# Kernel optimization log

Measured on AMD Instinct MI355X. Metric: run time of the kernel, lower is better.

Reference implementation:

```python
import jax, jax.numpy as jnp
import numpy as np

N, P, D = 262144, 128, 64
EPS = 1e-5
NEG = -1e30


def setup_inputs() -> dict:
    key = jax.random.key(0)
    ks = jax.random.split(key, 12)
    feature = jax.random.normal(ks[0], (N, D), jnp.float32)
    feature_geo = jax.random.normal(ks[1], (N, D), jnp.float32)
    xyz = jax.random.uniform(ks[2], (N, 3), jnp.float32)
    centers = jax.random.uniform(ks[3], (3,), jnp.float32)
    plane_center = jax.random.uniform(ks[4], (P, 3), jnp.float32)
    nrm = jax.random.normal(ks[5], (P, 3), jnp.float32)
    plane_normal = nrm / jnp.linalg.norm(nrm, axis=1, keepdims=True)
    lo = 0.3 * jax.random.uniform(ks[6], (P, 3), jnp.float32)
    hi = 0.5 + 0.5 * jax.random.uniform(ks[7], (P, 3), jnp.float32)
    # exactly two active axes per plane (one axis of the aabb is zeroed)
    ax = jnp.arange(P) % 3
    keep = (jnp.arange(3)[None, :] != ax[:, None]).astype(jnp.float32)
    plane_xyz_min = lo * keep
    plane_xyz_max = hi * keep
    w1 = 0.05 * jax.random.normal(ks[8], (2 * D, D), jnp.float32)
    b1 = jnp.zeros((D,), jnp.float32)
    w2 = 0.05 * jax.random.normal(ks[9], (D, D), jnp.float32)
    b2 = jnp.zeros((D,), jnp.float32)
    w3 = 0.05 * jax.random.normal(ks[10], (D, 1), jnp.float32)
    b3 = jnp.zeros((1,), jnp.float32)
    g1 = jnp.ones((D,), jnp.float32); be1 = jnp.zeros((D,), jnp.float32)
    m1 = jnp.zeros((D,), jnp.float32); v1 = jnp.ones((D,), jnp.float32)
    g2 = jnp.ones((D,), jnp.float32); be2 = jnp.zeros((D,), jnp.float32)
    m2 = jnp.zeros((D,), jnp.float32); v2 = jnp.ones((D,), jnp.float32)
    return dict(feature=feature, feature_geo=feature_geo, xyz=xyz, centers=centers,
                plane_center=plane_center, plane_normal=plane_normal,
                plane_xyz_min=plane_xyz_min, plane_xyz_max=plane_xyz_max,
                w1=w1, b1=b1, g1=g1, be1=be1, m1=m1, v1=v1,
                w2=w2, b2=b2, g2=g2, be2=be2, m2=m2, v2=v2,
                w3=w3, b3=b3)


def _bn(x, g, b, m, v):
    return (x - m) * (g * jax.lax.rsqrt(v + EPS)) + b


def reference(feature, feature_geo, xyz, centers, plane_center, plane_normal,
              plane_xyz_min, plane_xyz_max, w1, b1, g1, be1, m1, v1,
              w2, b2, g2, be2, m2, v2, w3, b3):
    clouds = xyz + centers                                   # [N,3]
    f = jnp.concatenate([feature, feature_geo], axis=1)      # [N,2D]
    # 1x1 conv MLP == per-point matmul (fc1 -> fc2 with BN+ReLU, fc3)
    h1 = jax.nn.relu(_bn(f @ w1 + b1, g1, be1, m1, v1))      # [N,D]
    h2 = jax.nn.relu(_bn(h1 @ w2 + b2, g2, be2, m2, v2))     # [N,D]
    scores = jax.nn.relu(h2 @ w3 + b3)[:, 0]                 # [N]
    # per-plane aabb mask over the two active axes (xyz_max != 0)
    active = plane_xyz_max != 0                              # [P,3]
    in_rng = (clouds[None] >= plane_xyz_min[:, None]) & (clouds[None] < plane_xyz_max[:, None])
    range_mask = jnp.all(in_rng | ~active[:, None, :], axis=-1)   # [P,N]
    # point-to-plane distance: |(clouds - center) . normal|
    dots = clouds @ plane_normal.T                           # [N,P]
    offs = jnp.sum(plane_center * plane_normal, axis=1)      # [P]
    dist = jnp.abs(dots - offs[None, :]).T                   # [P,N]
    mask = range_mask & (dist < 0.1)                         # [P,N]
    sig = jax.nn.sigmoid(scores)                             # [N]
    on_mask = mask & (sig > 0.5)[None, :]
    off_mask = mask & (sig <= 0.5)[None, :]

    def pool(m):  # masked max-pool of fc2 features over points of one plane
        val = jnp.max(jnp.where(m[:, None], h2, NEG), axis=0)     # [D]
        return jnp.where(jnp.any(m), val, 0.0)

    on_feat = jax.lax.map(pool, on_mask)                     # [P,D]
    off_feat = jax.lax.map(pool, off_mask)                   # [P,D]
    scores_masked = jnp.where(mask, scores[None, :], 0.0)    # [P,N]
    return scores_masked, mask, on_mask, off_mask, on_feat, off_feat
```

## Files before the change

kernel.cpp:

```cpp
#include <hip/hip_runtime.h>
#include <hip/hip_bf16.h>
#include <math.h>

#define NPTS 262144
#define NP   128
#define DD   64
#define NWORDS (NPTS / 64)

__global__ __launch_bounds__(256) void prep_kernel(
    const float* __restrict__ plane_center, const float* __restrict__ plane_normal,
    const float* __restrict__ pmin, const float* __restrict__ pmax,
    float* __restrict__ packed, float* __restrict__ out_feats)
{
    const int t = threadIdx.x;
    out_feats[blockIdx.x * 256 + t] = 0.0f;
    if (blockIdx.x == 0 && t < NP) {
        float n0 = plane_normal[t*3+0], n1 = plane_normal[t*3+1], n2 = plane_normal[t*3+2];
        float c0 = plane_center[t*3+0], c1 = plane_center[t*3+1], c2 = plane_center[t*3+2];
        float off = (c0*n0 + c1*n1) + c2*n2;
        float4* pp = reinterpret_cast<float4*>(packed) + t * 3;
        pp[0] = make_float4(n0, n1, n2, off);
        pp[1] = make_float4(pmin[t*3+0], pmin[t*3+1], pmin[t*3+2], 0.0f);
        pp[2] = make_float4(pmax[t*3+0], pmax[t*3+1], pmax[t*3+2], 0.0f);
    }
}

__global__ __launch_bounds__(256) void mlp1_kernel(
    const float* __restrict__ feature, const float* __restrict__ feature_geo,
    const float* __restrict__ w1, const float* __restrict__ b1,
    const float* __restrict__ g1, const float* __restrict__ be1,
    const float* __restrict__ m1, const float* __restrict__ v1,
    float* __restrict__ h1_out)
{
    const int n = blockIdx.x * 256 + threadIdx.x;
    float acc[DD];
#pragma unroll
    for (int j = 0; j < DD; ++j) acc[j] = 0.0f;

    const float4* fA = reinterpret_cast<const float4*>(feature) + (size_t)n * 16;
#pragma unroll 1
    for (int q = 0; q < 16; ++q) {
        const float4 fv = fA[q];
        const float* wr = w1 + q * 4 * DD;
#pragma unroll
        for (int j = 0; j < DD; ++j) acc[j] = fmaf(fv.x, wr[j], acc[j]);
#pragma unroll
        for (int j = 0; j < DD; ++j) acc[j] = fmaf(fv.y, wr[DD + j], acc[j]);
#pragma unroll
        for (int j = 0; j < DD; ++j) acc[j] = fmaf(fv.z, wr[2 * DD + j], acc[j]);
#pragma unroll
        for (int j = 0; j < DD; ++j) acc[j] = fmaf(fv.w, wr[3 * DD + j], acc[j]);
    }
    const float4* fB = reinterpret_cast<const float4*>(feature_geo) + (size_t)n * 16;
    const float* w1b = w1 + DD * DD;
#pragma unroll 1
    for (int q = 0; q < 16; ++q) {
        const float4 fv = fB[q];
        const float* wr = w1b + q * 4 * DD;
#pragma unroll
        for (int j = 0; j < DD; ++j) acc[j] = fmaf(fv.x, wr[j], acc[j]);
#pragma unroll
        for (int j = 0; j < DD; ++j) acc[j] = fmaf(fv.y, wr[DD + j], acc[j]);
#pragma unroll
        for (int j = 0; j < DD; ++j) acc[j] = fmaf(fv.z, wr[2 * DD + j], acc[j]);
#pragma unroll
        for (int j = 0; j < DD; ++j) acc[j] = fmaf(fv.w, wr[3 * DD + j], acc[j]);
    }
#pragma unroll
    for (int j = 0; j < DD; ++j) {
        float sc = g1[j] * (1.0f / sqrtf(v1[j] + 1e-5f));
        float h  = fmaf(acc[j] + b1[j] - m1[j], sc, be1[j]);
        acc[j] = fmaxf(h, 0.0f);
    }
    float4* o = reinterpret_cast<float4*>(h1_out) + (size_t)n * 16;
#pragma unroll
    for (int q = 0; q < 16; ++q)
        o[q] = make_float4(acc[4*q+0], acc[4*q+1], acc[4*q+2], acc[4*q+3]);
}

__global__ __launch_bounds__(256) void mlp2_kernel(
    const float* __restrict__ h1_in,
    const float* __restrict__ w2, const float* __restrict__ b2,
    const float* __restrict__ g2, const float* __restrict__ be2,
    const float* __restrict__ m2, const float* __restrict__ v2,
    const float* __restrict__ w3, const float* __restrict__ b3,
    float* __restrict__ h2_out, float* __restrict__ scores_out)
{
    const int n = blockIdx.x * 256 + threadIdx.x;
    float acc[DD];
#pragma unroll
    for (int j = 0; j < DD; ++j) acc[j] = 0.0f;

    const float4* fA = reinterpret_cast<const float4*>(h1_in) + (size_t)n * 16;
#pragma unroll 1
    for (int q = 0; q < 16; ++q) {
        const float4 fv = fA[q];
        const float* wr = w2 + q * 4 * DD;
#pragma unroll
        for (int j = 0; j < DD; ++j) acc[j] = fmaf(fv.x, wr[j], acc[j]);
#pragma unroll
        for (int j = 0; j < DD; ++j) acc[j] = fmaf(fv.y, wr[DD + j], acc[j]);
#pragma unroll
        for (int j = 0; j < DD; ++j) acc[j] = fmaf(fv.z, wr[2 * DD + j], acc[j]);
#pragma unroll
        for (int j = 0; j < DD; ++j) acc[j] = fmaf(fv.w, wr[3 * DD + j], acc[j]);
    }
    float s = 0.0f;
#pragma unroll
    for (int j = 0; j < DD; ++j) {
        float sc = g2[j] * (1.0f / sqrtf(v2[j] + 1e-5f));
        float h  = fmaf(acc[j] + b2[j] - m2[j], sc, be2[j]);
        h = fmaxf(h, 0.0f);
        acc[j] = h;
        s = fmaf(h, w3[j], s);
    }
    s += b3[0];
    float4* o = reinterpret_cast<float4*>(h2_out) + (size_t)n * 16;
#pragma unroll
    for (int q = 0; q < 16; ++q)
        o[q] = make_float4(acc[4*q+0], acc[4*q+1], acc[4*q+2], acc[4*q+3]);
    scores_out[n] = fmaxf(s, 0.0f);
}

__global__ __launch_bounds__(256) void mask_kernel(
    const float* __restrict__ xyz, const float* __restrict__ centers,
    const float* __restrict__ packed,
    const float* __restrict__ scores,
    float* __restrict__ out_sm, float* __restrict__ out_mask,
    float* __restrict__ out_on, float* __restrict__ out_off,
    unsigned long long* __restrict__ hitOn, unsigned long long* __restrict__ hitOff)
{
    const int t = threadIdx.x;
    const int n = blockIdx.x * 256 + t;
    const float c0 = xyz[n*3+0] + centers[0];
    const float c1 = xyz[n*3+1] + centers[1];
    const float c2 = xyz[n*3+2] + centers[2];
    const float s  = scores[n];
    const bool on  = (0.5f + 0.5f * tanhf(0.5f * s)) > 0.5f;
    const int lane = t & 63;
    const int word = n >> 6;

    const float4* pp = reinterpret_cast<const float4*>(packed);
#pragma unroll 1
    for (int p = 0; p < NP; ++p) {
        float4 nrm = pp[p*3+0];
        float4 mn  = pp[p*3+1];
        float4 mx  = pp[p*3+2];
        float d = fabsf(fmaf(c2, nrm.z, fmaf(c1, nrm.y, c0 * nrm.x)) - nrm.w);
        bool ok0 = (mx.x == 0.0f) | ((c0 >= mn.x) & (c0 < mx.x));
        bool ok1 = (mx.y == 0.0f) | ((c1 >= mn.y) & (c1 < mx.y));
        bool ok2 = (mx.z == 0.0f) | ((c2 >= mn.z) & (c2 < mx.z));
        bool mk  = ok0 & ok1 & ok2 & (d < 0.1f);
        size_t idx = (size_t)p * NPTS + n;
        out_sm[idx]   = mk ? s : 0.0f;
        out_mask[idx] = mk ? 1.0f : 0.0f;
        bool mon  = mk & on;
        bool moff = mk & (!on);
        out_on[idx]  = mon  ? 1.0f : 0.0f;
        out_off[idx] = moff ? 1.0f : 0.0f;
        unsigned long long bOn  = __ballot(mon);
        unsigned long long bOff = __ballot(moff);
        if (lane == 0) {
            hitOn [(size_t)p * NWORDS + word] = bOn;
            hitOff[(size_t)p * NWORDS + word] = bOff;
        }
    }
}

__global__ __launch_bounds__(256) void pool_kernel(
    const float* __restrict__ h2,
    const unsigned long long* __restrict__ hitOn,
    const unsigned long long* __restrict__ hitOff,
    int* __restrict__ out_feats_i)
{
    __shared__ float tile[128 * DD];
    __shared__ unsigned long long bm[2][NP][2];
    const int t = threadIdx.x;
    const int lane = t & 63;
    const int wv = t >> 6;

    float accOn[32], accOff[32];
#pragma unroll
    for (int i = 0; i < 32; ++i) { accOn[i] = 0.0f; accOff[i] = 0.0f; }

    for (int cc = 0; cc < 4; ++cc) {
        const int chunk = blockIdx.x * 4 + cc;
        const int base  = chunk * 128;
        const float4* src = reinterpret_cast<const float4*>(h2 + (size_t)base * DD);
        float4* dst = reinterpret_cast<float4*>(tile);
#pragma unroll
        for (int q = 0; q < 8; ++q) dst[t + q * 256] = src[t + q * 256];
        {
            const int p = t & 127;
            const int half = t >> 7;
            const unsigned long long* hsrc = half ? hitOff : hitOn;
            const int w0 = chunk * 2;
            bm[half][p][0] = hsrc[(size_t)p * NWORDS + w0 + 0];
            bm[half][p][1] = hsrc[(size_t)p * NWORDS + w0 + 1];
        }
        __syncthreads();

#pragma unroll
        for (int i = 0; i < 32; ++i) {
            const int p = wv * 32 + i;
            unsigned long long m;
            m = bm[0][p][0];
            while (m) { int nn = __builtin_ctzll(m); m &= m - 1;
                        accOn[i]  = fmaxf(accOn[i],  tile[nn * DD + lane]); }
            m = bm[0][p][1];
            while (m) { int nn = __builtin_ctzll(m); m &= m - 1;
                        accOn[i]  = fmaxf(accOn[i],  tile[(64 + nn) * DD + lane]); }
            m = bm[1][p][0];
            while (m) { int nn = __builtin_ctzll(m); m &= m - 1;
                        accOff[i] = fmaxf(accOff[i], tile[nn * DD + lane]); }
            m = bm[1][p][1];
            while (m) { int nn = __builtin_ctzll(m); m &= m - 1;
                        accOff[i] = fmaxf(accOff[i], tile[(64 + nn) * DD + lane]); }
        }
        __syncthreads();
    }
#pragma unroll
    for (int i = 0; i < 32; ++i) {
        const int p = wv * 32 + i;
        if (accOn[i]  != 0.0f) atomicMax(&out_feats_i[p * DD + lane],            __float_as_int(accOn[i]));
        if (accOff[i] != 0.0f) atomicMax(&out_feats_i[NP * DD + p * DD + lane],  __float_as_int(accOff[i]));
    }
}

extern "C" void kernel_launch(void* const* d_in, const int* in_sizes, int n_in,
                              void* d_out, int out_size, void* d_ws, size_t ws_size,
                              hipStream_t stream) {
    const float* feature      = (const float*)d_in[0];
    const float* feature_geo  = (const float*)d_in[1];
    const float* xyz          = (const float*)d_in[2];
    const float* centers      = (const float*)d_in[3];
    const float* plane_center = (const float*)d_in[4];
    const float* plane_normal = (const float*)d_in[5];
    const float* pmin         = (const float*)d_in[6];
    const float* pmax         = (const float*)d_in[7];
    const float* w1 = (const float*)d_in[8];
    const float* b1 = (const float*)d_in[9];
    const float* g1 = (const float*)d_in[10];
    const float* be1 = (const float*)d_in[11];
    const float* m1 = (const float*)d_in[12];
    const float* v1 = (const float*)d_in[13];
    const float* w2 = (const float*)d_in[14];
    const float* b2 = (const float*)d_in[15];
    const float* g2 = (const float*)d_in[16];
    const float* be2 = (const float*)d_in[17];
    const float* m2 = (const float*)d_in[18];
    const float* v2 = (const float*)d_in[19];
    const float* w3 = (const float*)d_in[20];
    const float* b3 = (const float*)d_in[21];

    float* out = (float*)d_out;
    const size_t PN = (size_t)NP * NPTS;
    float* out_sm    = out;
    float* out_mask  = out + PN;
    float* out_on    = out + 2 * PN;
    float* out_off   = out + 3 * PN;
    float* out_feats = out + 4 * PN;

    float* h1     = (float*)d_ws;
    float* h2     = h1 + (size_t)NPTS * DD;
    float* scores = h2 + (size_t)NPTS * DD;
    unsigned long long* hitOn  = (unsigned long long*)(scores + NPTS);
    unsigned long long* hitOff = hitOn + (size_t)NP * NWORDS;
    float* packed = (float*)(hitOff + (size_t)NP * NWORDS);

    prep_kernel<<<64, 256, 0, stream>>>(
        plane_center, plane_normal, pmin, pmax, packed, out_feats);
    mlp1_kernel<<<NPTS / 256, 256, 0, stream>>>(
        feature, feature_geo, w1, b1, g1, be1, m1, v1, h1);
    mlp2_kernel<<<NPTS / 256, 256, 0, stream>>>(
        h1, w2, b2, g2, be2, m2, v2, w3, b3, h2, scores);
    mask_kernel<<<NPTS / 256, 256, 0, stream>>>(
        xyz, centers, packed, scores,
        out_sm, out_mask, out_on, out_off, hitOn, hitOff);
    pool_kernel<<<512, 256, 0, stream>>>(h2, hitOn, hitOff, (int*)out_feats);
}
```

Measured before the change: 869.4 us.

## Fuse both MLP layers and mask generation into a single per-point kernel

Merges the two MLP kernels and the mask kernel into one kernel, so the first hidden layer and the score stay in registers instead of passing through global memory. This removes a large intermediate write/read and two launches. The cost is higher register pressure from holding two 64-float arrays at once, which may cause spills or lower occupancy during the store-heavy mask loop.

```diff
diff --git a/kernel.cpp b/kernel.cpp
--- a/kernel.cpp
+++ b/kernel.cpp
@@ -25,85 +25,82 @@
     }
 }
 
-__global__ __launch_bounds__(256) void mlp1_kernel(
+__global__ __launch_bounds__(256) void fused_kernel(
     const float* __restrict__ feature, const float* __restrict__ feature_geo,
+    const float* __restrict__ xyz, const float* __restrict__ centers,
+    const float* __restrict__ packed,
     const float* __restrict__ w1, const float* __restrict__ b1,
     const float* __restrict__ g1, const float* __restrict__ be1,
     const float* __restrict__ m1, const float* __restrict__ v1,
-    float* __restrict__ h1_out)
-{
-    const int n = blockIdx.x * 256 + threadIdx.x;
-    float acc[DD];
-#pragma unroll
-    for (int j = 0; j < DD; ++j) acc[j] = 0.0f;
-
-    const float4* fA = reinterpret_cast<const float4*>(feature) + (size_t)n * 16;
-#pragma unroll 1
-    for (int q = 0; q < 16; ++q) {
-        const float4 fv = fA[q];
-        const float* wr = w1 + q * 4 * DD;
-#pragma unroll
-        for (int j = 0; j < DD; ++j) acc[j] = fmaf(fv.x, wr[j], acc[j]);
-#pragma unroll
-        for (int j = 0; j < DD; ++j) acc[j] = fmaf(fv.y, wr[DD + j], acc[j]);
-#pragma unroll
-        for (int j = 0; j < DD; ++j) acc[j] = fmaf(fv.z, wr[2 * DD + j], acc[j]);
-#pragma unroll
-        for (int j = 0; j < DD; ++j) acc[j] = fmaf(fv.w, wr[3 * DD + j], acc[j]);
-    }
-    const float4* fB = reinterpret_cast<const float4*>(feature_geo) + (size_t)n * 16;
-    const float* w1b = w1 + DD * DD;
-#pragma unroll 1
-    for (int q = 0; q < 16; ++q) {
-        const float4 fv = fB[q];
-        const float* wr = w1b + q * 4 * DD;
-#pragma unroll
-        for (int j = 0; j < DD; ++j) acc[j] = fmaf(fv.x, wr[j], acc[j]);
-#pragma unroll
-        for (int j = 0; j < DD; ++j) acc[j] = fmaf(fv.y, wr[DD + j], acc[j]);
-#pragma unroll
-        for (int j = 0; j < DD; ++j) acc[j] = fmaf(fv.z, wr[2 * DD + j], acc[j]);
-#pragma unroll
-        for (int j = 0; j < DD; ++j) acc[j] = fmaf(fv.w, wr[3 * DD + j], acc[j]);
-    }
-#pragma unroll
-    for (int j = 0; j < DD; ++j) {
-        float sc = g1[j] * (1.0f / sqrtf(v1[j] + 1e-5f));
-        float h  = fmaf(acc[j] + b1[j] - m1[j], sc, be1[j]);
-        acc[j] = fmaxf(h, 0.0f);
-    }
-    float4* o = reinterpret_cast<float4*>(h1_out) + (size_t)n * 16;
-#pragma unroll
-    for (int q = 0; q < 16; ++q)
-        o[q] = make_float4(acc[4*q+0], acc[4*q+1], acc[4*q+2], acc[4*q+3]);
-}
-
-__global__ __launch_bounds__(256) void mlp2_kernel(
-    const float* __restrict__ h1_in,
     const float* __restrict__ w2, const float* __restrict__ b2,
     const float* __restrict__ g2, const float* __restrict__ be2,
     const float* __restrict__ m2, const float* __restrict__ v2,
     const float* __restrict__ w3, const float* __restrict__ b3,
-    float* __restrict__ h2_out, float* __restrict__ scores_out)
+    float* __restrict__ h2_out,
+    float* __restrict__ out_sm, float* __restrict__ out_mask,
+    float* __restrict__ out_on, float* __restrict__ out_off,
+    unsigned long long* __restrict__ hitOn, unsigned long long* __restrict__ hitOff)
 {
-    const int n = blockIdx.x * 256 + threadIdx.x;
+    const int t = threadIdx.x;
+    const int n = blockIdx.x * 256 + t;
+
+    const float c0 = xyz[n*3+0] + centers[0];
+    const float c1 = xyz[n*3+1] + centers[1];
+    const float c2 = xyz[n*3+2] + centers[2];
+
     float acc[DD];
 #pragma unroll
     for (int j = 0; j < DD; ++j) acc[j] = 0.0f;
 
-    const float4* fA = reinterpret_cast<const float4*>(h1_in) + (size_t)n * 16;
+    const float4* fA = reinterpret_cast<const float4*>(feature) + (size_t)n * 16;
 #pragma unroll 1
     for (int q = 0; q < 16; ++q) {
         const float4 fv = fA[q];
+        const float* wr = w1 + q * 4 * DD;
+#pragma unroll
+        for (int j = 0; j < DD; ++j) acc[j] = fmaf(fv.x, wr[j], acc[j]);
+#pragma unroll
+        for (int j = 0; j < DD; ++j) acc[j] = fmaf(fv.y, wr[DD + j], acc[j]);
+#pragma unroll
+        for (int j = 0; j < DD; ++j) acc[j] = fmaf(fv.z, wr[2 * DD + j], acc[j]);
+#pragma unroll
+        for (int j = 0; j < DD; ++j) acc[j] = fmaf(fv.w, wr[3 * DD + j], acc[j]);
+    }
+    const float4* fB = reinterpret_cast<const float4*>(feature_geo) + (size_t)n * 16;
+    const float* w1b = w1 + DD * DD;
+#pragma unroll 1
+    for (int q = 0; q < 16; ++q) {
+        const float4 fv = fB[q];
+        const float* wr = w1b + q * 4 * DD;
+#pragma unroll
+        for (int j = 0; j < DD; ++j) acc[j] = fmaf(fv.x, wr[j], acc[j]);
+#pragma unroll
+        for (int j = 0; j < DD; ++j) acc[j] = fmaf(fv.y, wr[DD + j], acc[j]);
+#pragma unroll
+        for (int j = 0; j < DD; ++j) acc[j] = fmaf(fv.z, wr[2 * DD + j], acc[j]);
+#pragma unroll
+        for (int j = 0; j < DD; ++j) acc[j] = fmaf(fv.w, wr[3 * DD + j], acc[j]);
+    }
+    float h1[DD];
+#pragma unroll
+    for (int j = 0; j < DD; ++j) {
+        float sc = g1[j] * (1.0f / sqrtf(v1[j] + 1e-5f));
+        float h  = fmaf(acc[j] + b1[j] - m1[j], sc, be1[j]);
+        h1[j] = fmaxf(h, 0.0f);
+        acc[j] = 0.0f;
+    }
+#pragma unroll 1
+    for (int q = 0; q < 16; ++q) {
+        const float fx = h1[4*q+0], fy = h1[4*q+1], fz = h1[4*q+2], fw = h1[4*q+3];
         const float* wr = w2 + q * 4 * DD;
 #pragma unroll
-        for (int j = 0; j < DD; ++j) acc[j] = fmaf(fv.x, wr[j], acc[j]);
-#pragma unroll
-        for (int j = 0; j < DD; ++j) acc[j] = fmaf(fv.y, wr[DD + j], acc[j]);
-#pragma unroll
-        for (int j = 0; j < DD; ++j) acc[j] = fmaf(fv.z, wr[2 * DD + j], acc[j]);
-#pragma unroll
-        for (int j = 0; j < DD; ++j) acc[j] = fmaf(fv.w, wr[3 * DD + j], acc[j]);
+        for (int j = 0; j < DD; ++j) acc[j] = fmaf(fx, wr[j], acc[j]);
+#pragma unroll
+        for (int j = 0; j < DD; ++j) acc[j] = fmaf(fy, wr[DD + j], acc[j]);
+#pragma unroll
+        for (int j = 0; j < DD; ++j) acc[j] = fmaf(fz, wr[2 * DD + j], acc[j]);
+#pragma unroll
+        for (int j = 0; j < DD; ++j) acc[j] = fmaf(fw, wr[3 * DD + j], acc[j]);
     }
     float s = 0.0f;
 #pragma unroll
@@ -115,28 +112,14 @@
         s = fmaf(h, w3[j], s);
     }
     s += b3[0];
+    const float score = fmaxf(s, 0.0f);
+
     float4* o = reinterpret_cast<float4*>(h2_out) + (size_t)n * 16;
 #pragma unroll
     for (int q = 0; q < 16; ++q)
         o[q] = make_float4(acc[4*q+0], acc[4*q+1], acc[4*q+2], acc[4*q+3]);
-    scores_out[n] = fmaxf(s, 0.0f);
-}
-
-__global__ __launch_bounds__(256) void mask_kernel(
-    const float* __restrict__ xyz, const float* __restrict__ centers,
-    const float* __restrict__ packed,
-    const float* __restrict__ scores,
-    float* __restrict__ out_sm, float* __restrict__ out_mask,
-    float* __restrict__ out_on, float* __restrict__ out_off,
-    unsigned long long* __restrict__ hitOn, unsigned long long* __restrict__ hitOff)
-{
-    const int t = threadIdx.x;
-    const int n = blockIdx.x * 256 + t;
-    const float c0 = xyz[n*3+0] + centers[0];
-    const float c1 = xyz[n*3+1] + centers[1];
-    const float c2 = xyz[n*3+2] + centers[2];
-    const float s  = scores[n];
-    const bool on  = (0.5f + 0.5f * tanhf(0.5f * s)) > 0.5f;
+
+    const bool on  = (0.5f + 0.5f * tanhf(0.5f * score)) > 0.5f;
     const int lane = t & 63;
     const int word = n >> 6;
 
@@ -152,7 +135,7 @@
         bool ok2 = (mx.z == 0.0f) | ((c2 >= mn.z) & (c2 < mx.z));
         bool mk  = ok0 & ok1 & ok2 & (d < 0.1f);
         size_t idx = (size_t)p * NPTS + n;
-        out_sm[idx]   = mk ? s : 0.0f;
+        out_sm[idx]   = mk ? score : 0.0f;
         out_mask[idx] = mk ? 1.0f : 0.0f;
         bool mon  = mk & on;
         bool moff = mk & (!on);
@@ -261,21 +244,16 @@
     float* out_off   = out + 3 * PN;
     float* out_feats = out + 4 * PN;
 
-    float* h1     = (float*)d_ws;
-    float* h2     = h1 + (size_t)NPTS * DD;
-    float* scores = h2 + (size_t)NPTS * DD;
-    unsigned long long* hitOn  = (unsigned long long*)(scores + NPTS);
+    float* h2     = (float*)d_ws;
+    unsigned long long* hitOn  = (unsigned long long*)(h2 + (size_t)NPTS * DD);
     unsigned long long* hitOff = hitOn + (size_t)NP * NWORDS;
     float* packed = (float*)(hitOff + (size_t)NP * NWORDS);
 
     prep_kernel<<<64, 256, 0, stream>>>(
         plane_center, plane_normal, pmin, pmax, packed, out_feats);
-    mlp1_kernel<<<NPTS / 256, 256, 0, stream>>>(
-        feature, feature_geo, w1, b1, g1, be1, m1, v1, h1);
-    mlp2_kernel<<<NPTS / 256, 256, 0, stream>>>(
-        h1, w2, b2, g2, be2, m2, v2, w3, b3, h2, scores);
-    mask_kernel<<<NPTS / 256, 256, 0, stream>>>(
-        xyz, centers, packed, scores,
-        out_sm, out_mask, out_on, out_off, hitOn, hitOff);
+    fused_kernel<<<NPTS / 256, 256, 0, stream>>>(
+        feature, feature_geo, xyz, centers, packed,
+        w1, b1, g1, be1, m1, v1, w2, b2, g2, be2, m2, v2, w3, b3,
+        h2, out_sm, out_mask, out_on, out_off, hitOn, hitOff);
     pool_kernel<<<512, 256, 0, stream>>>(h2, hitOn, hitOff, (int*)out_feats);
 }
```

Measured after the change: 842.5 us. -3.1%, faster.
